# Performance work log

Measured on AMD Instinct MI355X. Metric: run time of the kernel, lower is better.

## Reference

```python
import jax, jax.numpy as jnp
import numpy as np

B, N, D = 16, 512, 12
HID, HEADS = 32, 4
C = HID // HEADS  # per-head channels = 8


def setup_inputs() -> dict:
    key = jax.random.key(0)
    ks = jax.random.split(key, 12)
    s = 0.1
    return {
        "x": jax.random.normal(ks[0], (B, N, D), dtype=jnp.float32),
        "adj": jax.random.randint(ks[1], (B, N, N), 0, 2, dtype=jnp.int32),
        # node_proj: Linear(D, HID)
        "Wp": jax.random.normal(ks[2], (HID, D), dtype=jnp.float32) * s,
        "bp": jax.random.normal(ks[3], (HID,), dtype=jnp.float32) * s,
        # GATConv lin: Linear(HID, HEADS*C, bias=False)
        "Wg": jax.random.normal(ks[4], (HEADS * C, HID), dtype=jnp.float32) * s,
        "att_src": jax.random.normal(ks[5], (HEADS, C), dtype=jnp.float32) * s,
        "att_dst": jax.random.normal(ks[6], (HEADS, C), dtype=jnp.float32) * s,
        "bias_g": jax.random.normal(ks[7], (HEADS * C,), dtype=jnp.float32) * s,
        # edge_mlp: Linear(2*HID, HID) -> ReLU -> Linear(HID, 1) -> Sigmoid
        "W1": jax.random.normal(ks[8], (HID, 2 * HID), dtype=jnp.float32) * s,
        "b1": jax.random.normal(ks[9], (HID,), dtype=jnp.float32) * s,
        "w2": jax.random.normal(ks[10], (HID,), dtype=jnp.float32) * s,
        "b2": jax.random.normal(ks[11], (1,), dtype=jnp.float32) * s,
    }


def reference(x, adj, Wp, bp, Wg, att_src, att_dst, bias_g, W1, b1, w2, b2):
    Bq, Nq, _ = x.shape
    adj_b = adj != 0
    eye = jnp.eye(Nq, dtype=bool)

    # node_proj + ReLU
    h = jax.nn.relu(jnp.einsum('bnd,hd->bnh', x, Wp) + bp)  # [B,N,HID]

    # GATConv (PyG semantics): messages flow src=i (row) -> dst=j (col),
    # self-loops removed then re-added => diagonal forced on.
    g = jnp.einsum('bnd,kd->bnk', h, Wg).reshape(Bq, Nq, HEADS, C)  # [B,N,H,C]
    a_s = jnp.einsum('bnhc,hc->bnh', g, att_src)  # [B,N,H]
    a_d = jnp.einsum('bnhc,hc->bnh', g, att_dst)  # [B,N,H]
    logits = jax.nn.leaky_relu(a_s[:, :, None, :] + a_d[:, None, :, :], 0.2)  # [B,i,j,H]
    mask_sl = adj_b | eye
    logits = jnp.where(mask_sl[..., None], logits, -1e9)
    alpha = jax.nn.softmax(logits, axis=1)  # softmax over source i per target j
    h_gnn = jnp.einsum('bijh,bihc->bjhc', alpha, g).reshape(Bq, Nq, HEADS * C) + bias_g

    # edge MLP on all (i,j) pairs: cat([h_i, h_j]) -> split W1
    W1i, W1j = W1[:, :HID], W1[:, HID:]
    ti = jnp.einsum('bnd,hd->bnh', h_gnn, W1i)  # [B,N,HID] (row / i part)
    tj = jnp.einsum('bnd,hd->bnh', h_gnn, W1j)  # [B,N,HID] (col / j part)
    hidden = jax.nn.relu(ti[:, :, None, :] + tj[:, None, :, :] + b1)  # [B,N,N,HID]
    score = jax.nn.sigmoid(jnp.einsum('bijh,h->bij', hidden, w2) + b2[0])

    out_mask = adj_b & ~eye
    return jnp.where(out_mask, score, jnp.float32(0.0))
```

## Files before the change

kernel.cpp:

```cpp
#include <hip/hip_runtime.h>
#include <cstdint>

#define Bq 16
#define Nq 512
#define Dq 12
#define HID 32
#define HEADS 4
#define Cq 8

#define OFF_G     0u
#define OFF_AS    262144u
#define OFF_AD    294912u
#define OFF_TIT   327680u
#define OFF_TJBT  589824u
#define OFF_PACK  851968u

__global__ __launch_bounds__(256) void k0_node(
    const float* __restrict__ x, const float* __restrict__ Wp, const float* __restrict__ bp,
    const float* __restrict__ Wg, const float* __restrict__ att_src,
    const float* __restrict__ att_dst, float* __restrict__ ws) {
    __shared__ float xs[8 * Dq];
    __shared__ float hs[8][HID];
    int n_sub = threadIdx.x >> 5;
    int k = threadIdx.x & 31;
    int node0 = blockIdx.x * 8;
    if (threadIdx.x < 8 * Dq) xs[threadIdx.x] = x[(size_t)node0 * Dq + threadIdx.x];
    __syncthreads();
    float s = bp[k];
#pragma unroll
    for (int d = 0; d < Dq; d++) s = fmaf(Wp[k * Dq + d], xs[n_sub * Dq + d], s);
    hs[n_sub][k] = s > 0.f ? s : 0.f;
    __syncthreads();
    float g = 0.f;
#pragma unroll
    for (int d = 0; d < HID; d++) g = fmaf(Wg[k * HID + d], hs[n_sub][d], g);
    int nid = node0 + n_sub;
    ws[OFF_G + (size_t)nid * HID + k] = g;
    float ss = g * att_src[k];
    float sd = g * att_dst[k];
#pragma unroll
    for (int off = 1; off < 8; off <<= 1) {
        ss += __shfl_xor(ss, off);
        sd += __shfl_xor(sd, off);
    }
    if ((k & 7) == 0) {
        int h = k >> 3;
        ws[OFF_AS + (size_t)nid * HEADS + h] = ss;
        ws[OFF_AD + (size_t)nid * HEADS + h] = sd;
    }
}

__global__ __launch_bounds__(256, 2) void k1_fused(
    const int* __restrict__ adj, const float* __restrict__ bias_g,
    const float* __restrict__ W1, const float* __restrict__ b1,
    float* __restrict__ ws) {
    int b = blockIdx.y;
    int j0 = blockIdx.x * 16;
    int t = threadIdx.x;
    int jl = t & 15;
    int ig = t >> 4;
    int j = j0 + jl;

    __shared__ float smem[6176];
    float* red = smem;
    float* hgs = smem + 2880;
    float* W1s = smem + 3456;
    float* tjs = smem + 5632;

    float4 adv = *(const float4*)(ws + OFF_AD + ((size_t)b * Nq + j) * HEADS);

    const float* Gb = ws + OFF_G + (size_t)b * Nq * HID;
    const float* Ab = ws + OFF_AS + (size_t)b * Nq * HEADS;
    int ii_s = t >> 2, q_s = t & 3;

    float4 ga, gb2;
    float av;
    {
        const float* src = Gb + (size_t)ii_s * HID + q_s * 8;
        ga = *(const float4*)src;
        gb2 = *(const float4*)(src + 4);
        av = Ab[t];
        *(float4*)&smem[ii_s * 36 + q_s * 8] = ga;
        *(float4*)&smem[ii_s * 36 + q_s * 8 + 4] = gb2;
        smem[4608 + t] = av;
    }
    const int* adjp = adj + ((size_t)b * Nq + ig) * Nq + j;
    int cur[4], nxt[4];
#pragma unroll
    for (int kk = 0; kk < 4; kk++) cur[kk] = adjp[(size_t)(16 * kk) * Nq];

    float lsum[HEADS] = {0.f, 0.f, 0.f, 0.f};
    float acc[HEADS][Cq] = {};
    uint32_t mask = 0;

    for (int c = 0; c < 8; c++) {
        __syncthreads();
        const float* gsc = (c & 1) ? smem + 2304 : smem;
        const float* asc = (c & 1) ? smem + 4864 : smem + 4608;
        if (c < 7) {
            const float* src = Gb + (size_t)((c + 1) * 64 + ii_s) * HID + q_s * 8;
            ga = *(const float4*)src;
            gb2 = *(const float4*)(src + 4);
            av = Ab[(c + 1) * 256 + t];
#pragma unroll
            for (int kk = 0; kk < 4; kk++)
                nxt[kk] = adjp[(size_t)(64 * (c + 1) + 16 * kk) * Nq];
        }
#pragma unroll
        for (int kk = 0; kk < 4; kk++) {
            int m = 4 * c + kk;
            int i = 16 * m + ig;
            int a = cur[kk];
            bool msk = (a != 0) || (i == j);
            mask |= (uint32_t)(a != 0) << m;
            int ii = 16 * kk + ig;
            float4 asv = *(const float4*)&asc[ii * 4];
            const float* gr = &gsc[ii * 36];
            float zs[HEADS] = {asv.x + adv.x, asv.y + adv.y, asv.z + adv.z, asv.w + adv.w};
#pragma unroll
            for (int h = 0; h < HEADS; h++) {
                float z = zs[h];
                float lk = z > 0.f ? z : 0.2f * z;
                float e = msk ? __expf(lk) : 0.f;
                lsum[h] += e;
                float4 g0 = *(const float4*)(gr + h * 8);
                float4 g1 = *(const float4*)(gr + h * 8 + 4);
                acc[h][0] = fmaf(e, g0.x, acc[h][0]);
                acc[h][1] = fmaf(e, g0.y, acc[h][1]);
                acc[h][2] = fmaf(e, g0.z, acc[h][2]);
                acc[h][3] = fmaf(e, g0.w, acc[h][3]);
                acc[h][4] = fmaf(e, g1.x, acc[h][4]);
                acc[h][5] = fmaf(e, g1.y, acc[h][5]);
                acc[h][6] = fmaf(e, g1.z, acc[h][6]);
                acc[h][7] = fmaf(e, g1.w, acc[h][7]);
            }
        }
        if (c < 7) {
            float* gsn = (c & 1) ? smem : smem + 2304;
            float* asn = (c & 1) ? smem + 4608 : smem + 4864;
            *(float4*)&gsn[ii_s * 36 + q_s * 8] = ga;
            *(float4*)&gsn[ii_s * 36 + q_s * 8 + 4] = gb2;
            asn[t] = av;
#pragma unroll
            for (int kk = 0; kk < 4; kk++) cur[kk] = nxt[kk];
        }
    }

    ((uint32_t*)(ws + OFF_PACK))[((size_t)b * Nq + j) * 16 + ig] = mask;

    __syncthreads();

    {
        const float4* src = (const float4*)W1;
        for (int k = t; k < 512; k += 256) {
            int h = k >> 4, q = k & 15;
            *(float4*)&W1s[h * 68 + q * 4] = src[k];
        }
    }
    int w = t >> 6;
    auto dump = [&](int r, float v) {
        v += __shfl_xor(v, 16);
        v += __shfl_xor(v, 32);
        if ((t & 63) < 16) red[(r * 16 + jl) * 5 + w] = v;
    };
#pragma unroll
    for (int h = 0; h < HEADS; h++) dump(h, lsum[h]);
#pragma unroll
    for (int h = 0; h < HEADS; h++)
#pragma unroll
        for (int cc = 0; cc < Cq; cc++) dump(4 + h * 8 + cc, acc[h][cc]);
    __syncthreads();
    for (int o = t; o < 576; o += 256) {
        float* p = &red[o * 5];
        p[4] = (p[0] + p[1]) + (p[2] + p[3]);
    }
    __syncthreads();
    for (int o = t; o < 512; o += 256) {
        int d = o >> 4, jj = o & 15;
        float s = red[((4 + d) * 16 + jj) * 5 + 4];
        float l = red[((d >> 3) * 16 + jj) * 5 + 4];
        hgs[jj * 36 + d] = s * __builtin_amdgcn_rcpf(l) + bias_g[d];
    }
    __syncthreads();
    {
        int tg = t >> 4;
        float si0 = 0.f, sj0 = 0.f, si1 = 0.f, sj1 = 0.f;
        const float* w0 = &W1s[tg * 68];
        const float* w1 = &W1s[(tg + 16) * 68];
        const float* hr = &hgs[jl * 36];
#pragma unroll
        for (int d = 0; d < HID; d++) {
            float hv = hr[d];
            si0 = fmaf(hv, w0[d], si0);
            sj0 = fmaf(hv, w0[32 + d], sj0);
            si1 = fmaf(hv, w1[d], si1);
            sj1 = fmaf(hv, w1[32 + d], sj1);
        }
        ws[OFF_TIT + ((size_t)b * HID + tg) * Nq + j] = si0;
        ws[OFF_TIT + ((size_t)b * HID + tg + 16) * Nq + j] = si1;
        tjs[tg * 17 + jl] = sj0 + b1[tg];
        tjs[(tg + 16) * 17 + jl] = sj1 + b1[tg + 16];
    }
    __syncthreads();
    for (int o = t; o < 512; o += 256) {
        int jj = o >> 5, h = o & 31;
        ws[OFF_TJBT + ((size_t)b * Nq + j0 + jj) * HID + h] = tjs[h * 17 + jj];
    }
}

__global__ __launch_bounds__(256) void k3_score(const float* __restrict__ w2_p,
                                                const float* __restrict__ b2_p,
                                                const float* __restrict__ ws,
                                                float* __restrict__ out) {
    int b = blockIdx.y;
    int i0 = blockIdx.x * 16;
    int j = threadIdx.x;
    __shared__ float tisT[16 * 36];
    {
        int h = threadIdx.x >> 4, ii = threadIdx.x & 15;
        tisT[ii * 36 + h] = ws[OFF_TIT + ((size_t)b * HID + h) * Nq + i0 + ii];
        tisT[ii * 36 + h + 16] = ws[OFF_TIT + ((size_t)b * HID + h + 16) * Nq + i0 + ii];
    }
    float4 ta[8], tb[8];
    const float* rA = ws + OFF_TJBT + ((size_t)b * Nq + j) * HID;
    const float* rB = rA + (size_t)256 * HID;
#pragma unroll
    for (int q = 0; q < 8; q++) {
        ta[q] = *(const float4*)(rA + q * 4);
        tb[q] = *(const float4*)(rB + q * 4);
    }
    float w2l[HID];
#pragma unroll
    for (int h = 0; h < HID; h++) w2l[h] = w2_p[h];
    float b2 = b2_p[0];
    const uint32_t* mrow = (const uint32_t*)(ws + OFF_PACK) + ((size_t)b * Nq + j) * 16;
    uint4 mAv[4], mBv[4];
#pragma unroll
    for (int q = 0; q < 4; q++) {
        mAv[q] = ((const uint4*)mrow)[q];
        mBv[q] = ((const uint4*)(mrow + 256 * 16))[q];
    }
    int bit = i0 >> 4;
    __syncthreads();
#pragma unroll
    for (int ii = 0; ii < 16; ii++) {
        int i = i0 + ii;
        uint32_t mA = (ii & 3) == 0 ? mAv[ii >> 2].x : (ii & 3) == 1 ? mAv[ii >> 2].y
                    : (ii & 3) == 2 ? mAv[ii >> 2].z : mAv[ii >> 2].w;
        uint32_t mB = (ii & 3) == 0 ? mBv[ii >> 2].x : (ii & 3) == 1 ? mBv[ii >> 2].y
                    : (ii & 3) == 2 ? mBv[ii >> 2].z : mBv[ii >> 2].w;
        bool onA = (((mA >> bit) & 1u) != 0) && (i != j);
        bool onB = (((mB >> bit) & 1u) != 0) && (i != j + 256);
        float sA = b2, sB = b2;
#pragma unroll
        for (int q = 0; q < 8; q++) {
            float4 tq = *(const float4*)&tisT[ii * 36 + q * 4];
#pragma unroll
            for (int e = 0; e < 4; e++) {
                float ti = (e == 0) ? tq.x : (e == 1) ? tq.y : (e == 2) ? tq.z : tq.w;
                float tjA = (e == 0) ? ta[q].x : (e == 1) ? ta[q].y : (e == 2) ? ta[q].z : ta[q].w;
                float tjB = (e == 0) ? tb[q].x : (e == 1) ? tb[q].y : (e == 2) ? tb[q].z : tb[q].w;
                float tA = ti + tjA;
                tA = tA > 0.f ? tA : 0.f;
                sA = fmaf(tA, w2l[q * 4 + e], sA);
                float tB = ti + tjB;
                tB = tB > 0.f ? tB : 0.f;
                sB = fmaf(tB, w2l[q * 4 + e], sB);
            }
        }
        float scA = __builtin_amdgcn_rcpf(1.f + __expf(-sA));
        float scB = __builtin_amdgcn_rcpf(1.f + __expf(-sB));
        out[((size_t)b * Nq + i) * Nq + j] = onA ? scA : 0.f;
        out[((size_t)b * Nq + i) * Nq + j + 256] = onB ? scB : 0.f;
    }
}

extern "C" void kernel_launch(void* const* d_in, const int* in_sizes, int n_in,
                              void* d_out, int out_size, void* d_ws, size_t ws_size,
                              hipStream_t stream) {
    const float* x       = (const float*)d_in[0];
    const int*   adj     = (const int*)d_in[1];
    const float* Wp      = (const float*)d_in[2];
    const float* bp      = (const float*)d_in[3];
    const float* Wg      = (const float*)d_in[4];
    const float* att_src = (const float*)d_in[5];
    const float* att_dst = (const float*)d_in[6];
    const float* bias_g  = (const float*)d_in[7];
    const float* W1      = (const float*)d_in[8];
    const float* b1      = (const float*)d_in[9];
    const float* w2      = (const float*)d_in[10];
    const float* b2      = (const float*)d_in[11];
    float* out = (float*)d_out;
    float* ws = (float*)d_ws;
    (void)in_sizes; (void)n_in; (void)out_size; (void)ws_size;

    k0_node<<<dim3(1024), dim3(256), 0, stream>>>(x, Wp, bp, Wg, att_src, att_dst, ws);
    k1_fused<<<dim3(Nq / 16, Bq), dim3(256), 0, stream>>>(adj, bias_g, W1, b1, ws);
    k3_score<<<dim3(32, Bq), dim3(256), 0, stream>>>(w2, b2, ws, out);
}
```

Before: 128.5 us.

## Compute two targets per thread in GAT aggregation, use exp2 with prescaled logits

```diff
diff --git a/kernel.cpp b/kernel.cpp
--- a/kernel.cpp
+++ b/kernel.cpp
@@ -7,6 +7,7 @@
 #define HID 32
 #define HEADS 4
 #define Cq 8
+#define LOG2E 1.44269504088896f
 
 #define OFF_G     0u
 #define OFF_AS    262144u
@@ -45,8 +46,8 @@
     }
     if ((k & 7) == 0) {
         int h = k >> 3;
-        ws[OFF_AS + (size_t)nid * HEADS + h] = ss;
-        ws[OFF_AD + (size_t)nid * HEADS + h] = sd;
+        ws[OFF_AS + (size_t)nid * HEADS + h] = ss * LOG2E;
+        ws[OFF_AD + (size_t)nid * HEADS + h] = sd * LOG2E;
     }
 }
 
@@ -57,17 +58,19 @@
     int b = blockIdx.y;
     int j0 = blockIdx.x * 16;
     int t = threadIdx.x;
-    int jl = t & 15;
-    int ig = t >> 4;
-    int j = j0 + jl;
-
-    __shared__ float smem[6176];
+    int jl2 = t & 7;
+    int ig = t >> 3;
+    int par = ig >> 4;
+
+    __shared__ float smem[6688];
     float* red = smem;
     float* hgs = smem + 2880;
     float* W1s = smem + 3456;
     float* tjs = smem + 5632;
-
-    float4 adv = *(const float4*)(ws + OFF_AD + ((size_t)b * Nq + j) * HEADS);
+    uint32_t* mskp = (uint32_t*)(smem + 6176);
+
+    float4 adv0 = *(const float4*)(ws + OFF_AD + ((size_t)b * Nq + j0 + jl2) * HEADS);
+    float4 adv1 = *(const float4*)(ws + OFF_AD + ((size_t)b * Nq + j0 + jl2 + 8) * HEADS);
 
     const float* Gb = ws + OFF_G + (size_t)b * Nq * HID;
     const float* Ab = ws + OFF_AS + (size_t)b * Nq * HEADS;
@@ -84,14 +87,16 @@
         *(float4*)&smem[ii_s * 36 + q_s * 8 + 4] = gb2;
         smem[4608 + t] = av;
     }
-    const int* adjp = adj + ((size_t)b * Nq + ig) * Nq + j;
-    int cur[4], nxt[4];
-#pragma unroll
-    for (int kk = 0; kk < 4; kk++) cur[kk] = adjp[(size_t)(16 * kk) * Nq];
-
-    float lsum[HEADS] = {0.f, 0.f, 0.f, 0.f};
-    float acc[HEADS][Cq] = {};
-    uint32_t mask = 0;
+    const int* adjp = adj + ((size_t)b * Nq + ig) * Nq + j0 + jl2;
+    int cur[2][2], nxt[2][2];
+#pragma unroll
+    for (int mi = 0; mi < 2; mi++)
+#pragma unroll
+        for (int js = 0; js < 2; js++) cur[mi][js] = adjp[(size_t)(32 * mi) * Nq + 8 * js];
+
+    float lsum[2][HEADS] = {};
+    float acc[2][HEADS][Cq] = {};
+    uint32_t mask0 = 0, mask1 = 0;
 
     for (int c = 0; c < 8; c++) {
         __syncthreads();
@@ -103,36 +108,52 @@
             gb2 = *(const float4*)(src + 4);
             av = Ab[(c + 1) * 256 + t];
 #pragma unroll
-            for (int kk = 0; kk < 4; kk++)
-                nxt[kk] = adjp[(size_t)(64 * (c + 1) + 16 * kk) * Nq];
-        }
-#pragma unroll
-        for (int kk = 0; kk < 4; kk++) {
-            int m = 4 * c + kk;
-            int i = 16 * m + ig;
-            int a = cur[kk];
-            bool msk = (a != 0) || (i == j);
-            mask |= (uint32_t)(a != 0) << m;
-            int ii = 16 * kk + ig;
+            for (int mi = 0; mi < 2; mi++)
+#pragma unroll
+                for (int js = 0; js < 2; js++)
+                    nxt[mi][js] = adjp[(size_t)(64 * (c + 1) + 32 * mi) * Nq + 8 * js];
+        }
+#pragma unroll
+        for (int mi = 0; mi < 2; mi++) {
+            int m = 2 * c + mi;
+            int i = 32 * m + ig;
+            int ii = ig + 32 * mi;
+            bool c0 = (cur[mi][0] != 0), c1 = (cur[mi][1] != 0);
+            mask0 |= (uint32_t)c0 << (2 * m + par);
+            mask1 |= (uint32_t)c1 << (2 * m + par);
+            bool m0 = c0 || (i == j0 + jl2);
+            bool m1 = c1 || (i == j0 + jl2 + 8);
             float4 asv = *(const float4*)&asc[ii * 4];
             const float* gr = &gsc[ii * 36];
-            float zs[HEADS] = {asv.x + adv.x, asv.y + adv.y, asv.z + adv.z, asv.w + adv.w};
 #pragma unroll
             for (int h = 0; h < HEADS; h++) {
-                float z = zs[h];
-                float lk = z > 0.f ? z : 0.2f * z;
-                float e = msk ? __expf(lk) : 0.f;
-                lsum[h] += e;
+                float as_h = (h == 0) ? asv.x : (h == 1) ? asv.y : (h == 2) ? asv.z : asv.w;
+                float ad0 = (h == 0) ? adv0.x : (h == 1) ? adv0.y : (h == 2) ? adv0.z : adv0.w;
+                float ad1 = (h == 0) ? adv1.x : (h == 1) ? adv1.y : (h == 2) ? adv1.z : adv1.w;
+                float z0 = as_h + ad0, z1 = as_h + ad1;
+                float l0 = fmaxf(z0, 0.2f * z0), l1 = fmaxf(z1, 0.2f * z1);
+                float e0 = m0 ? __builtin_amdgcn_exp2f(l0) : 0.f;
+                float e1 = m1 ? __builtin_amdgcn_exp2f(l1) : 0.f;
+                lsum[0][h] += e0;
+                lsum[1][h] += e1;
                 float4 g0 = *(const float4*)(gr + h * 8);
                 float4 g1 = *(const float4*)(gr + h * 8 + 4);
-                acc[h][0] = fmaf(e, g0.x, acc[h][0]);
-                acc[h][1] = fmaf(e, g0.y, acc[h][1]);
-                acc[h][2] = fmaf(e, g0.z, acc[h][2]);
-                acc[h][3] = fmaf(e, g0.w, acc[h][3]);
-                acc[h][4] = fmaf(e, g1.x, acc[h][4]);
-                acc[h][5] = fmaf(e, g1.y, acc[h][5]);
-                acc[h][6] = fmaf(e, g1.z, acc[h][6]);
-                acc[h][7] = fmaf(e, g1.w, acc[h][7]);
+                acc[0][h][0] = fmaf(e0, g0.x, acc[0][h][0]);
+                acc[0][h][1] = fmaf(e0, g0.y, acc[0][h][1]);
+                acc[0][h][2] = fmaf(e0, g0.z, acc[0][h][2]);
+                acc[0][h][3] = fmaf(e0, g0.w, acc[0][h][3]);
+                acc[0][h][4] = fmaf(e0, g1.x, acc[0][h][4]);
+                acc[0][h][5] = fmaf(e0, g1.y, acc[0][h][5]);
+                acc[0][h][6] = fmaf(e0, g1.z, acc[0][h][6]);
+                acc[0][h][7] = fmaf(e0, g1.w, acc[0][h][7]);
+                acc[1][h][0] = fmaf(e1, g0.x, acc[1][h][0]);
+                acc[1][h][1] = fmaf(e1, g0.y, acc[1][h][1]);
+                acc[1][h][2] = fmaf(e1, g0.z, acc[1][h][2]);
+                acc[1][h][3] = fmaf(e1, g0.w, acc[1][h][3]);
+                acc[1][h][4] = fmaf(e1, g1.x, acc[1][h][4]);
+                acc[1][h][5] = fmaf(e1, g1.y, acc[1][h][5]);
+                acc[1][h][6] = fmaf(e1, g1.z, acc[1][h][6]);
+                acc[1][h][7] = fmaf(e1, g1.w, acc[1][h][7]);
             }
         }
         if (c < 7) {
@@ -142,14 +163,22 @@
             *(float4*)&gsn[ii_s * 36 + q_s * 8 + 4] = gb2;
             asn[t] = av;
 #pragma unroll
-            for (int kk = 0; kk < 4; kk++) cur[kk] = nxt[kk];
-        }
-    }
-
-    ((uint32_t*)(ws + OFF_PACK))[((size_t)b * Nq + j) * 16 + ig] = mask;
-
-    __syncthreads();
-
+            for (int mi = 0; mi < 2; mi++)
+#pragma unroll
+                for (int js = 0; js < 2; js++) cur[mi][js] = nxt[mi][js];
+        }
+    }
+
+    mskp[par * 256 + jl2 * 16 + (ig & 15)] = mask0;
+    mskp[par * 256 + (jl2 + 8) * 16 + (ig & 15)] = mask1;
+
+    __syncthreads();
+
+    {
+        int jl = t >> 4, w = t & 15;
+        uint32_t word = mskp[jl * 16 + w] | mskp[256 + jl * 16 + w];
+        ((uint32_t*)(ws + OFF_PACK))[((size_t)b * Nq + j0 + jl) * 16 + w] = word;
+    }
     {
         const float4* src = (const float4*)W1;
         for (int k = t; k < 512; k += 256) {
@@ -159,31 +188,38 @@
     }
     int w = t >> 6;
     auto dump = [&](int r, float v) {
+        v += __shfl_xor(v, 8);
         v += __shfl_xor(v, 16);
         v += __shfl_xor(v, 32);
-        if ((t & 63) < 16) red[(r * 16 + jl) * 5 + w] = v;
+        if ((t & 63) < 8) red[(r * 8 + jl2) * 5 + w] = v;
     };
 #pragma unroll
-    for (int h = 0; h < HEADS; h++) dump(h, lsum[h]);
-#pragma unroll
-    for (int h = 0; h < HEADS; h++)
-#pragma unroll
-        for (int cc = 0; cc < Cq; cc++) dump(4 + h * 8 + cc, acc[h][cc]);
+    for (int js = 0; js < 2; js++)
+#pragma unroll
+        for (int h = 0; h < HEADS; h++) dump(js * 36 + h, lsum[js][h]);
+#pragma unroll
+    for (int js = 0; js < 2; js++)
+#pragma unroll
+        for (int h = 0; h < HEADS; h++)
+#pragma unroll
+            for (int cc = 0; cc < Cq; cc++) dump(js * 36 + 4 + h * 8 + cc, acc[js][h][cc]);
     __syncthreads();
     for (int o = t; o < 576; o += 256) {
-        float* p = &red[o * 5];
-        p[4] = (p[0] + p[1]) + (p[2] + p[3]);
+        float* pp = &red[o * 5];
+        pp[4] = (pp[0] + pp[1]) + (pp[2] + pp[3]);
     }
     __syncthreads();
     for (int o = t; o < 512; o += 256) {
-        int d = o >> 4, jj = o & 15;
-        float s = red[((4 + d) * 16 + jj) * 5 + 4];
-        float l = red[((d >> 3) * 16 + jj) * 5 + 4];
-        hgs[jj * 36 + d] = s * __builtin_amdgcn_rcpf(l) + bias_g[d];
-    }
-    __syncthreads();
-    {
-        int tg = t >> 4;
+        int d = o >> 4, jl = o & 15;
+        int js = jl >> 3, j2 = jl & 7;
+        float s = red[((js * 36 + 4 + d) * 8 + j2) * 5 + 4];
+        float l = red[((js * 36 + (d >> 3)) * 8 + j2) * 5 + 4];
+        hgs[jl * 36 + d] = s * __builtin_amdgcn_rcpf(l) + bias_g[d];
+    }
+    __syncthreads();
+    {
+        int jl = t & 15, tg = t >> 4;
+        int j = j0 + jl;
         float si0 = 0.f, sj0 = 0.f, si1 = 0.f, sj1 = 0.f;
         const float* w0 = &W1s[tg * 68];
         const float* w1 = &W1s[(tg + 16) * 68];
@@ -231,8 +267,9 @@
     }
     float w2l[HID];
 #pragma unroll
-    for (int h = 0; h < HID; h++) w2l[h] = w2_p[h];
-    float b2 = b2_p[0];
+    for (int h = 0; h < HID; h++)
+        w2l[h] = __int_as_float(__builtin_amdgcn_readfirstlane(__float_as_int(w2_p[h])));
+    float b2 = __int_as_float(__builtin_amdgcn_readfirstlane(__float_as_int(b2_p[0])));
     const uint32_t* mrow = (const uint32_t*)(ws + OFF_PACK) + ((size_t)b * Nq + j) * 16;
     uint4 mAv[4], mBv[4];
 #pragma unroll
```

Measured after the change: 132.9 us. 1.03x slower.

## Halve per-block tile width in GAT and score kernels to double grid size

Applied to the files above, without the earlier changes.

```diff
diff --git a/kernel.cpp b/kernel.cpp
--- a/kernel.cpp
+++ b/kernel.cpp
@@ -50,25 +50,26 @@
     }
 }
 
-__global__ __launch_bounds__(256, 2) void k1_fused(
+__global__ __launch_bounds__(256, 4) void k1_fused(
     const int* __restrict__ adj, const float* __restrict__ bias_g,
     const float* __restrict__ W1, const float* __restrict__ b1,
     float* __restrict__ ws) {
     int b = blockIdx.y;
-    int j0 = blockIdx.x * 16;
+    int j0 = blockIdx.x * 8;
     int t = threadIdx.x;
-    int jl = t & 15;
-    int ig = t >> 4;
+    int jl = t & 7;
+    int ig = t >> 3;
+    int par = ig >> 4;
     int j = j0 + jl;
 
-    __shared__ float smem[6176];
+    __shared__ float smem[5376];
     float* red = smem;
-    float* hgs = smem + 2880;
-    float* W1s = smem + 3456;
-    float* tjs = smem + 5632;
+    float* hgs = smem + 1440;
+    float* W1s = smem + 1728;
+    float* tjs = smem + 3904;
+    uint32_t* mskp = (uint32_t*)(smem + 5120);
 
     float4 adv = *(const float4*)(ws + OFF_AD + ((size_t)b * Nq + j) * HEADS);
-
     const float* Gb = ws + OFF_G + (size_t)b * Nq * HID;
     const float* Ab = ws + OFF_AS + (size_t)b * Nq * HEADS;
     int ii_s = t >> 2, q_s = t & 3;
@@ -85,9 +86,9 @@
         smem[4608 + t] = av;
     }
     const int* adjp = adj + ((size_t)b * Nq + ig) * Nq + j;
-    int cur[4], nxt[4];
-#pragma unroll
-    for (int kk = 0; kk < 4; kk++) cur[kk] = adjp[(size_t)(16 * kk) * Nq];
+    int cur[2], nxt[2];
+    cur[0] = adjp[0];
+    cur[1] = adjp[(size_t)32 * Nq];
 
     float lsum[HEADS] = {0.f, 0.f, 0.f, 0.f};
     float acc[HEADS][Cq] = {};
@@ -102,18 +103,16 @@
             ga = *(const float4*)src;
             gb2 = *(const float4*)(src + 4);
             av = Ab[(c + 1) * 256 + t];
-#pragma unroll
-            for (int kk = 0; kk < 4; kk++)
-                nxt[kk] = adjp[(size_t)(64 * (c + 1) + 16 * kk) * Nq];
-        }
-#pragma unroll
-        for (int kk = 0; kk < 4; kk++) {
-            int m = 4 * c + kk;
-            int i = 16 * m + ig;
+            nxt[0] = adjp[(size_t)(64 * (c + 1)) * Nq];
+            nxt[1] = adjp[(size_t)(64 * (c + 1) + 32) * Nq];
+        }
+#pragma unroll
+        for (int kk = 0; kk < 2; kk++) {
+            int i = 64 * c + 32 * kk + ig;
             int a = cur[kk];
             bool msk = (a != 0) || (i == j);
-            mask |= (uint32_t)(a != 0) << m;
-            int ii = 16 * kk + ig;
+            mask |= (uint32_t)(a != 0) << (4 * c + 2 * kk + par);
+            int ii = 32 * kk + ig;
             float4 asv = *(const float4*)&asc[ii * 4];
             const float* gr = &gsc[ii * 36];
             float zs[HEADS] = {asv.x + adv.x, asv.y + adv.y, asv.z + adv.z, asv.w + adv.w};
@@ -141,15 +140,20 @@
             *(float4*)&gsn[ii_s * 36 + q_s * 8] = ga;
             *(float4*)&gsn[ii_s * 36 + q_s * 8 + 4] = gb2;
             asn[t] = av;
-#pragma unroll
-            for (int kk = 0; kk < 4; kk++) cur[kk] = nxt[kk];
-        }
-    }
-
-    ((uint32_t*)(ws + OFF_PACK))[((size_t)b * Nq + j) * 16 + ig] = mask;
-
-    __syncthreads();
-
+            cur[0] = nxt[0];
+            cur[1] = nxt[1];
+        }
+    }
+
+    mskp[par * 128 + jl * 16 + (ig & 15)] = mask;
+
+    __syncthreads();
+
+    if (t < 128) {
+        int jj = t >> 4, w = t & 15;
+        uint32_t word = mskp[jj * 16 + w] | mskp[128 + jj * 16 + w];
+        ((uint32_t*)(ws + OFF_PACK))[((size_t)b * Nq + j0 + jj) * 16 + w] = word;
+    }
     {
         const float4* src = (const float4*)W1;
         for (int k = t; k < 512; k += 256) {
@@ -159,9 +163,10 @@
     }
     int w = t >> 6;
     auto dump = [&](int r, float v) {
+        v += __shfl_xor(v, 8);
         v += __shfl_xor(v, 16);
         v += __shfl_xor(v, 32);
-        if ((t & 63) < 16) red[(r * 16 + jl) * 5 + w] = v;
+        if ((t & 63) < 8) red[(r * 8 + jl) * 5 + w] = v;
     };
 #pragma unroll
     for (int h = 0; h < HEADS; h++) dump(h, lsum[h]);
@@ -170,56 +175,50 @@
 #pragma unroll
         for (int cc = 0; cc < Cq; cc++) dump(4 + h * 8 + cc, acc[h][cc]);
     __syncthreads();
-    for (int o = t; o < 576; o += 256) {
-        float* p = &red[o * 5];
-        p[4] = (p[0] + p[1]) + (p[2] + p[3]);
-    }
-    __syncthreads();
-    for (int o = t; o < 512; o += 256) {
-        int d = o >> 4, jj = o & 15;
-        float s = red[((4 + d) * 16 + jj) * 5 + 4];
-        float l = red[((d >> 3) * 16 + jj) * 5 + 4];
+    for (int o = t; o < 288; o += 256) {
+        float* pp = &red[o * 5];
+        pp[4] = (pp[0] + pp[1]) + (pp[2] + pp[3]);
+    }
+    __syncthreads();
+    {
+        int d = t >> 3, jj = t & 7;
+        float s = red[((4 + d) * 8 + jj) * 5 + 4];
+        float l = red[((d >> 3) * 8 + jj) * 5 + 4];
         hgs[jj * 36 + d] = s * __builtin_amdgcn_rcpf(l) + bias_g[d];
     }
     __syncthreads();
     {
-        int tg = t >> 4;
-        float si0 = 0.f, sj0 = 0.f, si1 = 0.f, sj1 = 0.f;
+        int tg = t >> 3;
+        float si = 0.f, sj = 0.f;
         const float* w0 = &W1s[tg * 68];
-        const float* w1 = &W1s[(tg + 16) * 68];
         const float* hr = &hgs[jl * 36];
 #pragma unroll
         for (int d = 0; d < HID; d++) {
             float hv = hr[d];
-            si0 = fmaf(hv, w0[d], si0);
-            sj0 = fmaf(hv, w0[32 + d], sj0);
-            si1 = fmaf(hv, w1[d], si1);
-            sj1 = fmaf(hv, w1[32 + d], sj1);
-        }
-        ws[OFF_TIT + ((size_t)b * HID + tg) * Nq + j] = si0;
-        ws[OFF_TIT + ((size_t)b * HID + tg + 16) * Nq + j] = si1;
-        tjs[tg * 17 + jl] = sj0 + b1[tg];
-        tjs[(tg + 16) * 17 + jl] = sj1 + b1[tg + 16];
-    }
-    __syncthreads();
-    for (int o = t; o < 512; o += 256) {
-        int jj = o >> 5, h = o & 31;
-        ws[OFF_TJBT + ((size_t)b * Nq + j0 + jj) * HID + h] = tjs[h * 17 + jj];
+            si = fmaf(hv, w0[d], si);
+            sj = fmaf(hv, w0[32 + d], sj);
+        }
+        ws[OFF_TIT + ((size_t)b * HID + tg) * Nq + j] = si;
+        tjs[tg * 9 + jl] = sj + b1[tg];
+    }
+    __syncthreads();
+    {
+        int jj = t >> 5, h = t & 31;
+        ws[OFF_TJBT + ((size_t)b * Nq + j0 + jj) * HID + h] = tjs[h * 9 + jj];
     }
 }
 
-__global__ __launch_bounds__(256) void k3_score(const float* __restrict__ w2_p,
-                                                const float* __restrict__ b2_p,
-                                                const float* __restrict__ ws,
-                                                float* __restrict__ out) {
+__global__ __launch_bounds__(256, 4) void k3_score(const float* __restrict__ w2_p,
+                                                   const float* __restrict__ b2_p,
+                                                   const float* __restrict__ ws,
+                                                   float* __restrict__ out) {
     int b = blockIdx.y;
-    int i0 = blockIdx.x * 16;
+    int i0 = blockIdx.x * 8;
     int j = threadIdx.x;
-    __shared__ float tisT[16 * 36];
-    {
-        int h = threadIdx.x >> 4, ii = threadIdx.x & 15;
+    __shared__ float tisT[8 * 36];
+    {
+        int h = threadIdx.x >> 3, ii = threadIdx.x & 7;
         tisT[ii * 36 + h] = ws[OFF_TIT + ((size_t)b * HID + h) * Nq + i0 + ii];
-        tisT[ii * 36 + h + 16] = ws[OFF_TIT + ((size_t)b * HID + h + 16) * Nq + i0 + ii];
     }
     float4 ta[8], tb[8];
     const float* rA = ws + OFF_TJBT + ((size_t)b * Nq + j) * HID;
@@ -233,17 +232,18 @@
 #pragma unroll
     for (int h = 0; h < HID; h++) w2l[h] = w2_p[h];
     float b2 = b2_p[0];
-    const uint32_t* mrow = (const uint32_t*)(ws + OFF_PACK) + ((size_t)b * Nq + j) * 16;
-    uint4 mAv[4], mBv[4];
-#pragma unroll
-    for (int q = 0; q < 4; q++) {
+    const uint32_t* mrow = (const uint32_t*)(ws + OFF_PACK)
+                         + ((size_t)b * Nq + j) * 16 + (i0 & 8);
+    uint4 mAv[2], mBv[2];
+#pragma unroll
+    for (int q = 0; q < 2; q++) {
         mAv[q] = ((const uint4*)mrow)[q];
         mBv[q] = ((const uint4*)(mrow + 256 * 16))[q];
     }
     int bit = i0 >> 4;
     __syncthreads();
 #pragma unroll
-    for (int ii = 0; ii < 16; ii++) {
+    for (int ii = 0; ii < 8; ii++) {
         int i = i0 + ii;
         uint32_t mA = (ii & 3) == 0 ? mAv[ii >> 2].x : (ii & 3) == 1 ? mAv[ii >> 2].y
                     : (ii & 3) == 2 ? mAv[ii >> 2].z : mAv[ii >> 2].w;
@@ -295,6 +295,6 @@
     (void)in_sizes; (void)n_in; (void)out_size; (void)ws_size;
 
     k0_node<<<dim3(1024), dim3(256), 0, stream>>>(x, Wp, bp, Wg, att_src, att_dst, ws);
-    k1_fused<<<dim3(Nq / 16, Bq), dim3(256), 0, stream>>>(adj, bias_g, W1, b1, ws);
-    k3_score<<<dim3(32, Bq), dim3(256), 0, stream>>>(w2, b2, ws, out);
+    k1_fused<<<dim3(Nq / 8, Bq), dim3(256), 0, stream>>>(adj, bias_g, W1, b1, ws);
+    k3_score<<<dim3(64, Bq), dim3(256), 0, stream>>>(w2, b2, ws, out);
 }
```

New measurement: 133.4 us. 3.8% more time.
